# Performance work log

Hardware: AMD Instinct MI355X
Metric: run time of the kernel (lower is better)

The kernel has to match this reference:

```python
import math
import jax, jax.numpy as jnp
import numpy as np

NUM_PRE_NMS = 2000
NMS_THR = 0.7
MIN_SIZE = 16.0
LOG_MAX = math.log(1000.0 / 16)  # clamp on dh, dw as in the torch module

B, A, H, W = 8, 3, 200, 304
STRIDE = 4


def _make_anchors():
    # grid anchors, channel-last anchor ordering to match permute(0,2,3,1)
    sizes = np.array([32.0, 64.0, 128.0], dtype=np.float32)  # A sizes
    ys = (np.arange(H, dtype=np.float32) + 0.5) * STRIDE
    xs = (np.arange(W, dtype=np.float32) + 0.5) * STRIDE
    cy, cx = np.meshgrid(ys, xs, indexing="ij")  # [H,W]
    cx = cx[:, :, None]
    cy = cy[:, :, None]
    half = (sizes / 2.0)[None, None, :]  # [1,1,A]
    anc = np.stack([cx - half, cy - half, cx + half, cy + half], axis=-1)  # [H,W,A,4]
    anc = anc.reshape(-1, 4)  # [H*W*A, 4]
    anc = np.broadcast_to(anc[None], (B, anc.shape[0], 4)).copy()
    return jnp.asarray(anc)


def setup_inputs() -> dict:
    key = jax.random.key(0)
    k1, k2 = jax.random.split(key)
    cls_logits = jax.random.normal(k1, (B, A, H, W), dtype=jnp.float32)
    regs = jax.random.normal(k2, (B, 4 * A, H, W), dtype=jnp.float32) * 0.1
    anchors = _make_anchors()
    return {"cls_logits": cls_logits, "regs": regs, "anchors": anchors,
            "image_h": 800, "image_w": 1216}


def _box_iou(boxes):
    # boxes: [K,4] -> iou [K,K]
    x1, y1, x2, y2 = boxes[:, 0], boxes[:, 1], boxes[:, 2], boxes[:, 3]
    area = (x2 - x1) * (y2 - y1)
    ix1 = jnp.maximum(x1[:, None], x1[None, :])
    iy1 = jnp.maximum(y1[:, None], y1[None, :])
    ix2 = jnp.minimum(x2[:, None], x2[None, :])
    iy2 = jnp.minimum(y2[:, None], y2[None, :])
    iw = jnp.clip(ix2 - ix1, 0.0)
    ih = jnp.clip(iy2 - iy1, 0.0)
    inter = iw * ih
    union = area[:, None] + area[None, :] - inter
    return inter / jnp.maximum(union, 1e-6)


def _nms_one(boxes, valid):
    # boxes sorted by descending score; greedy suppression, fixed-size keep mask
    k = boxes.shape[0]
    iou = _box_iou(boxes)
    later = jnp.arange(k)

    def body(i, keep):
        sup = (iou[i] > NMS_THR) & keep[i] & (later > i)
        return keep & ~sup

    return jax.lax.fori_loop(0, k, body, valid)


def reference(cls_logits, regs, anchors, image_h, image_w):
    b = cls_logits.shape[0]
    # scores/regs in channel-last anchor order (matches permute(0,2,3,1))
    scores = jnp.transpose(cls_logits, (0, 2, 3, 1)).reshape(b, -1)       # [B,N]
    deltas = jnp.transpose(regs, (0, 2, 3, 1)).reshape(b, -1, 4)          # [B,N,4]
    n = scores.shape[1]
    k = min(NUM_PRE_NMS, n)

    top_scores, idx = jax.lax.top_k(scores, k)                            # [B,K]
    top_deltas = jnp.take_along_axis(deltas, idx[:, :, None], axis=1)     # [B,K,4]
    top_anchors = jnp.take_along_axis(anchors, idx[:, :, None], axis=1)   # [B,K,4]

    dx, dy = top_deltas[..., 0], top_deltas[..., 1]
    dh = jnp.minimum(top_deltas[..., 2], LOG_MAX)
    dw = jnp.minimum(top_deltas[..., 3], LOG_MAX)
    ah = top_anchors[..., 3] - top_anchors[..., 1]
    aw = top_anchors[..., 2] - top_anchors[..., 0]
    cx = aw / 2
    cy = ah / 2
    px = cx + dx * aw
    py = cy + dy * ah
    ph = jnp.exp(dh) * ah
    pw = jnp.exp(dw) * aw
    boxes = jnp.stack([px - pw / 2, py - ph / 2, px + pw / 2, py + ph / 2], axis=-1)  # [B,K,4]

    # size filter on clamped coords (as in _nms)
    w_img = jnp.float32(image_w)
    h_img = jnp.float32(image_h)
    bw = jnp.clip(boxes[..., 2], 0.0, w_img) - jnp.clip(boxes[..., 0], 0.0, w_img)
    bh = jnp.clip(boxes[..., 3], 0.0, h_img) - jnp.clip(boxes[..., 1], 0.0, h_img)
    valid = (bw >= MIN_SIZE) & (bh >= MIN_SIZE)

    keep = jax.vmap(_nms_one)(boxes, valid)                               # [B,K]
    out_boxes = boxes * keep[..., None].astype(boxes.dtype)
    return out_boxes, top_scores, keep
```

## Files before the change

### kernel.cpp

```cpp
#include <hip/hip_runtime.h>

#define HWSZ 60800
#define NA 3
#define NTOT 182400
#define KSEL 2000
#define CANDCAP 8192
#define NBATCH 8
#define GSPLIT 128
#define LOG_MAX_F 4.135166556742356f

#define OFF_H1    0
#define OFF_CCNT  65536
#define ZR_BYTES  65568
#define OFF_SEL   65568
#define OFF_BOX   65696
#define OFF_VALID 321696
#define OFF_SUP   385696
#define OFF_CAND  385696
#define OFF_SUPT  4481696


__device__ __forceinline__ unsigned int xform(float f) {
    unsigned int b = __float_as_uint(f);
    return b ^ ((unsigned int)((int)b >> 31) | 0x80000000u);
}

__device__ __forceinline__ void bar_lds() {
    asm volatile("s_waitcnt lgkmcnt(0)" ::: "memory");
    __builtin_amdgcn_s_barrier();
}

__global__ __launch_bounds__(256) void k_hist1(const float* __restrict__ cls,
                                               unsigned int* __restrict__ hist1) {
    int b = blockIdx.y, part = blockIdx.x, tid = threadIdx.x;
    __shared__ unsigned int h[2048];
    for (int i = tid; i < 2048; i += 256) h[i] = 0u;
    __syncthreads();
    const float4* base4 = (const float4*)(cls + (size_t)b * NTOT);
    const int n4 = NTOT / 4;
    int per = (n4 + GSPLIT - 1) / GSPLIT;
    int lo = part * per, hi = lo + per;
    if (hi > n4) hi = n4;
    for (int i = lo + tid; i < hi; i += 256) {
        float4 v = base4[i];
        atomicAdd(&h[xform(v.x) >> 21], 1u);
        atomicAdd(&h[xform(v.y) >> 21], 1u);
        atomicAdd(&h[xform(v.z) >> 21], 1u);
        atomicAdd(&h[xform(v.w) >> 21], 1u);
    }
    __syncthreads();
    unsigned int* gh = hist1 + b * 2048;
    for (int i = tid; i < 2048; i += 256)
        if (h[i]) atomicAdd(&gh[i], h[i]);
}

__global__ __launch_bounds__(1024) void k_scan1(const unsigned int* __restrict__ hist1,
                                                uint4* __restrict__ selinfo) {
    int b = blockIdx.x, tid = threadIdx.x;
    __shared__ unsigned int sa[2048], sb[2048];
    const unsigned int* h = hist1 + b * 2048;
    sa[tid] = h[tid];
    sa[tid + 1024] = h[tid + 1024];
    unsigned int* src = sa; unsigned int* dst = sb;
    for (int d = 1; d < 2048; d <<= 1) {
        __syncthreads();
        dst[tid] = src[tid] + ((tid + d < 2048) ? src[tid + d] : 0u);
        int i2 = tid + 1024;
        dst[i2] = src[i2] + ((i2 + d < 2048) ? src[i2 + d] : 0u);
        unsigned int* t = src; src = dst; dst = t;
    }
    __syncthreads();
    #pragma unroll
    for (int k = 0; k < 2; ++k) {
        int i = tid + k * 1024;
        unsigned int c = src[i];
        unsigned int cn = (i < 2047) ? src[i + 1] : 0u;
        if (c >= KSEL && cn < KSEL)
            selinfo[b] = make_uint4((unsigned int)i, cn, KSEL - cn, 0u);
    }
}

__global__ __launch_bounds__(256) void k_gather(const float* __restrict__ cls,
                                                const uint4* __restrict__ selinfo,
                                                unsigned long long* __restrict__ cand,
                                                unsigned int* __restrict__ ccnt) {
    int b = blockIdx.y, part = blockIdx.x, tid = threadIdx.x;
    unsigned int bin = selinfo[b].x;
    __shared__ unsigned long long lbuf[1024];
    __shared__ unsigned int lcnt, gbase;
    if (tid == 0) lcnt = 0u;
    __syncthreads();
    const float4* base4 = (const float4*)(cls + (size_t)b * NTOT);
    const int n4 = NTOT / 4;
    int per = (n4 + GSPLIT - 1) / GSPLIT;
    int lo = part * per, hi = lo + per;
    if (hi > n4) hi = n4;
    for (int i = lo + tid; i < hi; i += 256) {
        float4 v = base4[i];
        float vals[4] = {v.x, v.y, v.z, v.w};
        int idx0 = i * 4;
        #pragma unroll
        for (int q = 0; q < 4; ++q) {
            unsigned int u = xform(vals[q]);
            if ((u >> 21) >= bin) {
                int idx = idx0 + q;
                int a = idx / HWSZ;
                int hw = idx - a * HWSZ;
                unsigned int n = (unsigned int)(hw * NA + a);
                unsigned int pos = atomicAdd(&lcnt, 1u);
                if (pos < 1024u)
                    lbuf[pos] = ((unsigned long long)u << 32) | (unsigned long long)(~n);
            }
        }
    }
    __syncthreads();
    if (tid == 0) {
        unsigned int c = lcnt < 1024u ? lcnt : 1024u;
        gbase = atomicAdd(&ccnt[b], c);
    }
    __syncthreads();
    unsigned int c = lcnt < 1024u ? lcnt : 1024u;
    unsigned int gb = gbase;
    for (unsigned int i = tid; i < c; i += 256) {
        unsigned int p = gb + i;
        if (p < CANDCAP) cand[(size_t)b * CANDCAP + p] = lbuf[i];
    }
}

__global__ __launch_bounds__(256) void k_rank_decode(
        const unsigned long long* __restrict__ cand,
        const unsigned int* __restrict__ ccnt,
        const float* __restrict__ regs,
        const float* __restrict__ anchors,
        const int* __restrict__ img_h,
        const int* __restrict__ img_w,
        float* __restrict__ out_scores,
        float4* __restrict__ boxes_ws,
        unsigned int* __restrict__ valid_ws) {
    int b = blockIdx.y;
    int tid = threadIdx.x;
    unsigned int sc = ccnt[b];
    if (sc > CANDCAP) sc = CANDCAP;
    unsigned int kbase = blockIdx.x * 64;
    if (kbase >= sc) return;
    int ki = tid & 63;
    int q = tid >> 6;
    int lane = tid & 63;
    const unsigned long long* sb_ = cand + (size_t)b * CANDCAP;
    unsigned int r = kbase + (unsigned int)ki;
    unsigned long long mykey = (r < sc) ? sb_[r] : 0ULL;

    unsigned int qs = ((sc + 255u) >> 8) << 6;
    unsigned int lo = (unsigned int)q * qs;
    unsigned int hi = lo + qs;
    if (hi > sc) hi = sc;

    unsigned int cnt = 0u;
    for (unsigned int base = lo; base < hi; base += 64) {
        unsigned long long kj = 0ULL;
        if (base + (unsigned int)lane < hi) kj = sb_[base + lane];
        unsigned int klo = (unsigned int)kj;
        unsigned int khi = (unsigned int)(kj >> 32);
        #pragma unroll
        for (int t = 0; t < 64; ++t) {
            unsigned int lo_ = (unsigned int)__builtin_amdgcn_readlane((int)klo, t);
            unsigned int hi_ = (unsigned int)__builtin_amdgcn_readlane((int)khi, t);
            unsigned long long kt = ((unsigned long long)hi_ << 32) | (unsigned long long)lo_;
            cnt += (kt > mykey) ? 1u : 0u;
        }
    }
    __shared__ unsigned int cntsh[4][64];
    cntsh[q][ki] = cnt;
    __syncthreads();
    if (tid >= 64) return;
    unsigned int rank = cntsh[0][ki] + cntsh[1][ki] + cntsh[2][ki] + cntsh[3][ki];
    if (r >= sc || rank >= KSEL) return;

    int hv = img_h[0];
    int wv = img_w[0];
    float himg = (hv > 0 && hv < 100000) ? (float)hv : __int_as_float(hv);
    float wimg = (wv > 0 && wv < 100000) ? (float)wv : __int_as_float(wv);

    unsigned int u = (unsigned int)(mykey >> 32);
    unsigned int n = ~((unsigned int)mykey);
    unsigned int bits = (u & 0x80000000u) ? (u & 0x7FFFFFFFu) : ~u;
    float score = __uint_as_float(bits);
    int a = (int)(n % NA);
    int hw = (int)(n / NA);
    const float* rp = regs + ((size_t)b * (4 * NA) + 4 * a) * HWSZ + hw;
    float dx = rp[0 * HWSZ];
    float dy = rp[1 * HWSZ];
    float dh = rp[2 * HWSZ];
    float dw = rp[3 * HWSZ];
    const float* ap = anchors + ((size_t)b * NTOT + n) * 4;
    float ax1 = ap[0], ay1 = ap[1], ax2 = ap[2], ay2 = ap[3];
    float ahh = ay2 - ay1;
    float aww = ax2 - ax1;
    float cx = aww * 0.5f;
    float cy = ahh * 0.5f;
    float px = cx + dx * aww;
    float py = cy + dy * ahh;
    dh = fminf(dh, LOG_MAX_F);
    dw = fminf(dw, LOG_MAX_F);
    float ph = expf(dh) * ahh;
    float pw = expf(dw) * aww;
    float x1 = px - pw * 0.5f;
    float y1 = py - ph * 0.5f;
    float x2 = px + pw * 0.5f;
    float y2 = py + ph * 0.5f;
    float bwv = fminf(fmaxf(x2, 0.f), wimg) - fminf(fmaxf(x1, 0.f), wimg);
    float bhv = fminf(fmaxf(y2, 0.f), himg) - fminf(fmaxf(y1, 0.f), himg);
    unsigned int valid = (bwv >= 16.f && bhv >= 16.f) ? 1u : 0u;
    size_t o = (size_t)b * KSEL + rank;
    out_scores[o] = score;
    boxes_ws[o] = make_float4(x1, y1, x2, y2);
    valid_ws[o] = valid;
}

__global__ __launch_bounds__(256) void k_supmat(const float4* __restrict__ boxes_ws,
                                                unsigned long long* __restrict__ sup,
                                                unsigned long long* __restrict__ supT) {
    int ct = blockIdx.x;
    int rt = blockIdx.y;
    int b  = blockIdx.z;
    if (ct * 64 + 63 < rt * 256) return;
    int tid = threadIdx.x;
    __shared__ float4 colbox[64];
    int j0 = ct * 64;
    if (tid < 64) {
        int jl = j0 + tid;
        colbox[tid] = (jl < KSEL) ? boxes_ws[(size_t)b * KSEL + jl]
                                  : make_float4(0.f, 0.f, 0.f, 0.f);
    }
    __syncthreads();
    int i = rt * 256 + tid;
    if (i >= KSEL) return;
    float4 bi = boxes_ws[(size_t)b * KSEL + i];
    float area_i = (bi.z - bi.x) * (bi.w - bi.y);
    unsigned long long word = 0ULL;
    #pragma unroll 8
    for (int jj = 0; jj < 64; ++jj) {
        int j = j0 + jj;
        float4 bj = colbox[jj];
        float area_j = (bj.z - bj.x) * (bj.w - bj.y);
        float ix1 = fmaxf(bi.x, bj.x);
        float iy1 = fmaxf(bi.y, bj.y);
        float ix2 = fminf(bi.z, bj.z);
        float iy2 = fminf(bi.w, bj.w);
        float iw = fmaxf(ix2 - ix1, 0.f);
        float ih = fmaxf(iy2 - iy1, 0.f);
        float inter = iw * ih;
        float uni = area_i + area_j - inter;
        float iou = inter / fmaxf(uni, 1e-6f);
        bool s = (j > i) && (j < KSEL) && (iou > 0.7f);
        if (s) word |= (1ULL << jj);
    }
    if (ct >= (i >> 6))
        sup[((size_t)b * KSEL + i) * 32 + ct] = word;

    if (ct == rt * 4 + (tid >> 6)) {
        int lane = tid & 63;
        unsigned long long cm = 0ULL;
        #pragma unroll
        for (int j = 0; j < 64; ++j) {
            unsigned long long t = __ballot((word >> j) & 1ULL);
            if (lane == j) cm = t;
        }
        supT[((size_t)b * 32 + ct) * 64 + lane] = cm;
    }
}

#define LOAD_TILE(wnext, buf)                                                \
    {                                                                        \
        int w_ = (wnext);                                                    \
        _Pragma("unroll")                                                    \
        for (int k = 0; k < 4; ++k) {                                        \
            int lr_ = (tid >> 4) + k * 16;                                   \
            int grow_ = w_ * 64 + lr_;                                       \
            if (grow_ > KSEL - 1) grow_ = KSEL - 1;                          \
            int pp_ = (2 * p + 1 >= w_) ? p : 15;                            \
            buf[k] = srowp[(size_t)grow_ * 16 + pp_];                        \
        }                                                                    \
    }

#define PROCESS_TILE(w, buf)                                                 \
    {                                                                        \
        bar_lds();                                                           \
        int w_ = (w);                                                        \
        unsigned long long pend_ =                                           \
            ((unsigned long long)accw[w_ * 2 + 1] << 32)                     \
            | (unsigned long long)accw[w_ * 2];                              \
        unsigned long long cand_ = kws[w_] & ~pend_;                         \
        unsigned int clo_ = __builtin_amdgcn_readfirstlane((unsigned int)cand_);        \
        unsigned int chi_ = __builtin_amdgcn_readfirstlane((unsigned int)(cand_ >> 32));\
        unsigned long long cur_ = ((unsigned long long)chi_ << 32)           \
                                  | (unsigned long long)clo_;                \
        if (cur_) {                                                          \
            unsigned long long cmw_ = colT[w_ * 64 + lane];                  \
            unsigned long long k_ = cur_;                                    \
            for (;;) {                                                       \
                unsigned long long sup_ = __ballot((k_ & cmw_) != 0ULL);     \
                unsigned long long k2_ = cur_ & ~sup_;                       \
                if (k2_ == k_) break;                                        \
                k_ = k2_;                                                    \
            }                                                                \
            cur_ = k_;                                                       \
            if (tid == 0) fin[w_] = cur_;                                    \
            unsigned long long v0_ = 0ULL, v1_ = 0ULL;                       \
            _Pragma("unroll")                                                \
            for (int k = 0; k < 4; ++k) {                                    \
                int lr_ = (tid >> 4) + k * 16;                               \
                if ((cur_ >> lr_) & 1ULL) { v0_ |= buf[k].x; v1_ |= buf[k].y; } \
            }                                                                \
            v0_ |= __shfl_xor(v0_, 16, 64); v0_ |= __shfl_xor(v0_, 32, 64);  \
            v1_ |= __shfl_xor(v1_, 16, 64); v1_ |= __shfl_xor(v1_, 32, 64);  \
            if (lane < 16) {                                                 \
                int wd0_ = 2 * p;                                            \
                if (wd0_ > w_ && v0_) {                                      \
                    atomicOr(&accw[wd0_ * 2], (unsigned int)v0_);            \
                    atomicOr(&accw[wd0_ * 2 + 1], (unsigned int)(v0_ >> 32));\
                }                                                            \
                if (wd0_ + 1 > w_ && v1_) {                                  \
                    atomicOr(&accw[wd0_ * 2 + 2], (unsigned int)v1_);        \
                    atomicOr(&accw[wd0_ * 2 + 3], (unsigned int)(v1_ >> 32));\
                }                                                            \
            }                                                                \
        } else if (tid == 0) {                                               \
            fin[w_] = 0ULL;                                                  \
        }                                                                    \
    }

__global__ __launch_bounds__(256) void k_nms_scan(const unsigned long long* __restrict__ sup,
                                                  const unsigned long long* __restrict__ supT,
                                                  const unsigned int* __restrict__ valid_ws,
                                                  const float4* __restrict__ boxes_ws,
                                                  float* __restrict__ out_boxes,
                                                  float* __restrict__ out_keep) {
    int b = blockIdx.x;
    int tid = threadIdx.x;
    int lane = tid & 63;
    int p = tid & 15;
    __shared__ unsigned long long kws[32];
    __shared__ unsigned long long fin[32];
    __shared__ unsigned int accw[64];
    __shared__ unsigned long long colT[32 * 64];
    const ulonglong2* srowp = (const ulonglong2*)(sup + (size_t)b * KSEL * 32);

    {
        const unsigned long long* stb = supT + (size_t)b * 2048;
        #pragma unroll
        for (int k = 0; k < 8; ++k) {
            int i = tid + k * 256;
            colT[i] = stb[i];
        }
    }

    if (tid < 32) {
        unsigned long long kw = 0ULL;
        const uint4* vv = (const uint4*)(valid_ws + (size_t)b * KSEL);
        #pragma unroll 4
        for (int q = 0; q < 16; ++q) {
            uint4 x = vv[tid * 16 + q];
            int base = q * 4;
            if (x.x) kw |= 1ULL << (base + 0);
            if (x.y) kw |= 1ULL << (base + 1);
            if (x.z) kw |= 1ULL << (base + 2);
            if (x.w) kw |= 1ULL << (base + 3);
        }
        if (tid == 31) kw &= 0xFFFFULL;
        kws[tid] = kw;
    }
    if (tid < 64) accw[tid] = 0u;

    ulonglong2 A[4], B[4], C[4], D[4];
    LOAD_TILE(0, A);
    LOAD_TILE(1, B);
    LOAD_TILE(2, C);
    LOAD_TILE(3, D);

    for (int t = 0; t < 8; ++t) {
        int w = 4 * t;
        PROCESS_TILE(w, A);
        if (w + 4 < 32) LOAD_TILE(w + 4, A);
        PROCESS_TILE(w + 1, B);
        if (w + 5 < 32) LOAD_TILE(w + 5, B);
        PROCESS_TILE(w + 2, C);
        if (w + 6 < 32) LOAD_TILE(w + 6, C);
        PROCESS_TILE(w + 3, D);
        if (w + 7 < 32) LOAD_TILE(w + 7, D);
    }
    bar_lds();

    float4* ob4 = (float4*)out_boxes;
    for (int r = tid; r < KSEL; r += 256) {
        float kf = (float)((fin[r >> 6] >> (r & 63)) & 1ULL);
        size_t o = (size_t)b * KSEL + r;
        out_keep[o] = kf;
        float4 bx = boxes_ws[o];
        ob4[o] = make_float4(bx.x * kf, bx.y * kf, bx.z * kf, bx.w * kf);
    }
}

extern "C" void kernel_launch(void* const* d_in, const int* in_sizes, int n_in,
                              void* d_out, int out_size, void* d_ws, size_t ws_size,
                              hipStream_t stream) {
    const float* cls     = (const float*)d_in[0];
    const float* regs    = (const float*)d_in[1];
    const float* anchors = (const float*)d_in[2];
    const int*   img_h   = (const int*)d_in[3];
    const int*   img_w   = (const int*)d_in[4];

    float* out = (float*)d_out;
    float* out_boxes  = out;
    float* out_scores = out + 64000;
    float* out_keep   = out + 80000;

    char* ws = (char*)d_ws;
    unsigned int* hist1      = (unsigned int*)(ws + OFF_H1);
    unsigned int* ccnt       = (unsigned int*)(ws + OFF_CCNT);
    uint4* selinfo           = (uint4*)(ws + OFF_SEL);
    float4* boxes_ws         = (float4*)(ws + OFF_BOX);
    unsigned int* valid_ws   = (unsigned int*)(ws + OFF_VALID);
    unsigned long long* sup  = (unsigned long long*)(ws + OFF_SUP);
    unsigned long long* cand = (unsigned long long*)(ws + OFF_CAND);
    unsigned long long* supT = (unsigned long long*)(ws + OFF_SUPT);

    hipMemsetAsync(ws, 0, ZR_BYTES, stream);
    k_hist1<<<dim3(GSPLIT, NBATCH), 256, 0, stream>>>(cls, hist1);
    k_scan1<<<NBATCH, 1024, 0, stream>>>(hist1, selinfo);
    k_gather<<<dim3(GSPLIT, NBATCH), 256, 0, stream>>>(cls, selinfo, cand, ccnt);
    k_rank_decode<<<dim3(CANDCAP / 64, NBATCH), 256, 0, stream>>>(cand, ccnt, regs, anchors,
                                                                  img_h, img_w, out_scores,
                                                                  boxes_ws, valid_ws);
    k_supmat<<<dim3(32, 8, NBATCH), 256, 0, stream>>>(boxes_ws, sup, supT);
    k_nms_scan<<<NBATCH, 256, 0, stream>>>(sup, supT, valid_ws, boxes_ws, out_boxes, out_keep);
}
```

Measured before the change: 199.2 us.

## Fuse histogram scan into gather kernel and skip loads for suppressed rows

Removes the separate k_scan1 launch: every gather block now redundantly loads the 2048-bin histogram and does its own prefix scan in shared memory to find the threshold bin, saving a kernel launch and the selinfo round trip. In the NMS scan, tile loads now redirect rows that are already suppressed or invalid to a single shared row address, aiming to cut redundant global traffic. A barrier is added so kws/accw are visible before the first tile loads. The cost is 1024 blocks each repeating an 11-step scan over 2048 entries and extra shared-memory use per block.

```diff
diff --git a/kernel.cpp b/kernel.cpp
--- a/kernel.cpp
+++ b/kernel.cpp
@@ -12,12 +12,11 @@
 #define OFF_H1    0
 #define OFF_CCNT  65536
 #define ZR_BYTES  65568
-#define OFF_SEL   65568
-#define OFF_BOX   65696
-#define OFF_VALID 321696
-#define OFF_SUP   385696
-#define OFF_CAND  385696
-#define OFF_SUPT  4481696
+#define OFF_BOX   65568
+#define OFF_VALID 321568
+#define OFF_SUP   385568
+#define OFF_CAND  385568
+#define OFF_SUPT  4481568
 
 
 __device__ __forceinline__ unsigned int xform(float f) {
@@ -54,42 +53,43 @@
         if (h[i]) atomicAdd(&gh[i], h[i]);
 }
 
-__global__ __launch_bounds__(1024) void k_scan1(const unsigned int* __restrict__ hist1,
-                                                uint4* __restrict__ selinfo) {
-    int b = blockIdx.x, tid = threadIdx.x;
+__global__ __launch_bounds__(256) void k_gather(const float* __restrict__ cls,
+                                                const unsigned int* __restrict__ hist1,
+                                                unsigned long long* __restrict__ cand,
+                                                unsigned int* __restrict__ ccnt) {
+    int b = blockIdx.y, part = blockIdx.x, tid = threadIdx.x;
     __shared__ unsigned int sa[2048], sb[2048];
-    const unsigned int* h = hist1 + b * 2048;
-    sa[tid] = h[tid];
-    sa[tid + 1024] = h[tid + 1024];
+    __shared__ unsigned long long lbuf[1024];
+    __shared__ unsigned int lcnt, gbase, sbin;
+
+    const unsigned int* gh = hist1 + b * 2048;
+    #pragma unroll
+    for (int k = 0; k < 8; ++k) {
+        int i = tid + k * 256;
+        sa[i] = gh[i];
+    }
+    if (tid == 0) lcnt = 0u;
     unsigned int* src = sa; unsigned int* dst = sb;
     for (int d = 1; d < 2048; d <<= 1) {
         __syncthreads();
-        dst[tid] = src[tid] + ((tid + d < 2048) ? src[tid + d] : 0u);
-        int i2 = tid + 1024;
-        dst[i2] = src[i2] + ((i2 + d < 2048) ? src[i2 + d] : 0u);
+        #pragma unroll
+        for (int k = 0; k < 8; ++k) {
+            int i = tid + k * 256;
+            dst[i] = src[i] + ((i + d < 2048) ? src[i + d] : 0u);
+        }
         unsigned int* t = src; src = dst; dst = t;
     }
     __syncthreads();
     #pragma unroll
-    for (int k = 0; k < 2; ++k) {
-        int i = tid + k * 1024;
+    for (int k = 0; k < 8; ++k) {
+        int i = tid + k * 256;
         unsigned int c = src[i];
         unsigned int cn = (i < 2047) ? src[i + 1] : 0u;
-        if (c >= KSEL && cn < KSEL)
-            selinfo[b] = make_uint4((unsigned int)i, cn, KSEL - cn, 0u);
-    }
-}
-
-__global__ __launch_bounds__(256) void k_gather(const float* __restrict__ cls,
-                                                const uint4* __restrict__ selinfo,
-                                                unsigned long long* __restrict__ cand,
-                                                unsigned int* __restrict__ ccnt) {
-    int b = blockIdx.y, part = blockIdx.x, tid = threadIdx.x;
-    unsigned int bin = selinfo[b].x;
-    __shared__ unsigned long long lbuf[1024];
-    __shared__ unsigned int lcnt, gbase;
-    if (tid == 0) lcnt = 0u;
-    __syncthreads();
+        if (c >= KSEL && cn < KSEL) sbin = (unsigned int)i;
+    }
+    __syncthreads();
+    unsigned int bin = sbin;
+
     const float4* base4 = (const float4*)(cls + (size_t)b * NTOT);
     const int n4 = NTOT / 4;
     int per = (n4 + GSPLIT - 1) / GSPLIT;
@@ -273,11 +273,15 @@
 #define LOAD_TILE(wnext, buf)                                                \
     {                                                                        \
         int w_ = (wnext);                                                    \
+        unsigned long long pe_ =                                             \
+            ((unsigned long long)accw[w_ * 2 + 1] << 32)                     \
+            | (unsigned long long)accw[w_ * 2];                              \
+        unsigned long long est_ = kws[w_] & ~pe_;                            \
         _Pragma("unroll")                                                    \
         for (int k = 0; k < 4; ++k) {                                        \
             int lr_ = (tid >> 4) + k * 16;                                   \
             int grow_ = w_ * 64 + lr_;                                       \
-            if (grow_ > KSEL - 1) grow_ = KSEL - 1;                          \
+            if (!((est_ >> lr_) & 1ULL)) grow_ = w_ * 64;                    \
             int pp_ = (2 * p + 1 >= w_) ? p : 15;                            \
             buf[k] = srowp[(size_t)grow_ * 16 + pp_];                        \
         }                                                                    \
@@ -371,6 +375,7 @@
         kws[tid] = kw;
     }
     if (tid < 64) accw[tid] = 0u;
+    bar_lds();
 
     ulonglong2 A[4], B[4], C[4], D[4];
     LOAD_TILE(0, A);
@@ -418,7 +423,6 @@
     char* ws = (char*)d_ws;
     unsigned int* hist1      = (unsigned int*)(ws + OFF_H1);
     unsigned int* ccnt       = (unsigned int*)(ws + OFF_CCNT);
-    uint4* selinfo           = (uint4*)(ws + OFF_SEL);
     float4* boxes_ws         = (float4*)(ws + OFF_BOX);
     unsigned int* valid_ws   = (unsigned int*)(ws + OFF_VALID);
     unsigned long long* sup  = (unsigned long long*)(ws + OFF_SUP);
@@ -427,8 +431,7 @@
 
     hipMemsetAsync(ws, 0, ZR_BYTES, stream);
     k_hist1<<<dim3(GSPLIT, NBATCH), 256, 0, stream>>>(cls, hist1);
-    k_scan1<<<NBATCH, 1024, 0, stream>>>(hist1, selinfo);
-    k_gather<<<dim3(GSPLIT, NBATCH), 256, 0, stream>>>(cls, selinfo, cand, ccnt);
+    k_gather<<<dim3(GSPLIT, NBATCH), 256, 0, stream>>>(cls, hist1, cand, ccnt);
     k_rank_decode<<<dim3(CANDCAP / 64, NBATCH), 256, 0, stream>>>(cand, ccnt, regs, anchors,
                                                                   img_h, img_w, out_scores,
                                                                   boxes_ws, valid_ws);
```

Result: no change. 202.1 us (+1.5%).
